# Kernel optimization log

Hardware: AMD Instinct MI355X
Metric: run time of the kernel (lower is better)

Reference implementation:

```python
import jax, jax.numpy as jnp
import numpy as np

N = 50000
C_IN = 64
C_OUT = 64
K = 16
EPS = 1e-5


def _bn(x, g, b, m, v):
    # eval-mode BatchNorm1d over last dim
    return (x - m) * jax.lax.rsqrt(v + EPS) * g + b


def setup_inputs() -> dict:
    key = jax.random.key(0)
    ks = jax.random.split(key, 24)
    def lin(i, fan_in, fan_out):
        s = 1.0 / np.sqrt(fan_in)
        W = jax.random.uniform(ks[i], (fan_in, fan_out), jnp.float32, -s, s)
        b = jax.random.uniform(ks[i + 1], (fan_out,), jnp.float32, -s, s)
        return W, b
    Wq, bq = lin(0, C_IN, C_OUT)
    Wk, bk = lin(2, C_IN, C_OUT)
    Wv, bv = lin(4, C_IN, C_OUT)
    Wp, b_p = lin(6, 3, C_OUT)
    Wg1, bg1 = lin(8, C_OUT, C_OUT)
    Wg2, bg2 = lin(10, C_OUT, C_OUT)
    Wo, bo = lin(12, C_OUT, C_OUT)
    def bn_params(i):
        g = jax.random.uniform(ks[i], (C_OUT,), jnp.float32, 0.5, 1.5)
        b = jax.random.normal(ks[i + 1], (C_OUT,), jnp.float32) * 0.1
        m = jax.random.normal(ks[i + 2], (C_OUT,), jnp.float32) * 0.1
        v = jax.random.uniform(ks[i + 3], (C_OUT,), jnp.float32, 0.5, 1.5)
        return g, b, m, v
    bnp_g, bnp_b, bnp_m, bnp_v = bn_params(14)
    bng_g, bng_b, bng_m, bng_v = bn_params(18)
    points = jax.random.normal(ks[22], (N, 3), jnp.float32)
    features = jax.random.normal(ks[23], (N, C_IN), jnp.float32)
    grouped_indices = jax.random.randint(jax.random.fold_in(key, 7), (N, K), 0, N, jnp.int64 if jax.config.jax_enable_x64 else jnp.int32)
    return dict(points=points, features=features, grouped_indices=grouped_indices,
                Wq=Wq, bq=bq, Wk=Wk, bk=bk, Wv=Wv, bv=bv, Wp=Wp, b_p=b_p,
                bnp_g=bnp_g, bnp_b=bnp_b, bnp_m=bnp_m, bnp_v=bnp_v,
                Wg1=Wg1, bg1=bg1, bng_g=bng_g, bng_b=bng_b, bng_m=bng_m, bng_v=bng_v,
                Wg2=Wg2, bg2=bg2, Wo=Wo, bo=bo)


def reference(points, features, grouped_indices,
              Wq, bq, Wk, bk, Wv, bv, Wp, b_p,
              bnp_g, bnp_b, bnp_m, bnp_v,
              Wg1, bg1, bng_g, bng_b, bng_m, bng_v,
              Wg2, bg2, Wo, bo):
    q = features @ Wq + bq                      # (N, C)
    k = features @ Wk + bk
    v = features @ Wv + bv
    gpts = points[grouped_indices]              # (N, K, 3) gather
    gk = k[grouped_indices]                     # (N, K, C)
    gv = v[grouped_indices]                     # (N, K, C)
    rel = gpts - points[:, None, :]             # (N, K, 3)
    p = jax.nn.relu(_bn(rel @ Wp + b_p, bnp_g, bnp_b, bnp_m, bnp_v))  # (N, K, C)
    a = q[:, None, :] - gk + p                  # (N, K, C)
    h = jax.nn.relu(_bn(a @ Wg1 + bg1, bng_g, bng_b, bng_m, bng_v)) @ Wg2 + bg2
    attn = jax.nn.softmax(h, axis=1)            # softmax over neighbor axis
    out = jnp.sum((gv + p) * attn, axis=1) @ Wo + bo  # (N, C)
    return out
```

## Files before the change

### kernel.cpp

```cpp
#include <hip/hip_runtime.h>
#include <hip/hip_bf16.h>

#define EPSV 1e-5f
#define TW 4
#define TPW 8
#define SPD 76
#define WPD 68

typedef __attribute__((ext_vector_type(8))) short s8v;
typedef __attribute__((ext_vector_type(8))) unsigned short u8v;
typedef __attribute__((ext_vector_type(4))) unsigned short u4v;
typedef __attribute__((ext_vector_type(4))) float f4v;

struct InP {
  const float *points, *features; const int* gidx;
  const float *Wq,*bq,*Wk,*bk,*Wv,*bv,*Wp,*b_p;
  const float *bnp_g,*bnp_b,*bnp_m,*bnp_v;
  const float *Wg1,*bg1,*bng_g,*bng_b,*bng_m,*bng_v;
  const float *Wg2,*bg2,*Wo,*bo;
  float* out; int N;
};
struct WS {
  unsigned short *qW1;
  unsigned short *kvT;
  unsigned short *WAf, *Wkf, *Wvf, *W1f, *W2f, *Wof;
  unsigned short *Wpf;
  float *bq1F, *bpF, *bk1F;
};

__device__ __forceinline__ unsigned short f2bf(float x){
  __hip_bfloat16 h = __float2bfloat16(x);
  unsigned short u; __builtin_memcpy(&u, &h, 2); return u;
}
__device__ __forceinline__ float bf2f(unsigned short s){
  union{unsigned u; float f;} c; c.u = ((unsigned)s) << 16; return c.f;
}
__device__ __forceinline__ unsigned pk2(float x, float y){
  __hip_bfloat162 h = __float22bfloat162_rn(make_float2(x, y));
  unsigned u; __builtin_memcpy(&u, &h, 4); return u;
}
__device__ __forceinline__ s8v pack8(f4v x0, f4v x1){
  s8v r;
  ((unsigned*)&r)[0] = pk2(x0[0], x0[1]);
  ((unsigned*)&r)[1] = pk2(x0[2], x0[3]);
  ((unsigned*)&r)[2] = pk2(x1[0], x1[1]);
  ((unsigned*)&r)[3] = pk2(x1[2], x1[3]);
  return r;
}

__global__ void __launch_bounds__(256) prep_kernel(InP P, WS W){
  __shared__ __align__(16) float sWg1[64*WPD];
  __shared__ __align__(16) float sWq [64*WPD];
  __shared__ __align__(16) float sWk [64*WPD];
  const int tid = threadIdx.x;
  {
    int r = tid >> 2, c0 = (tid & 3) * 16;
    const f4v* g1 = (const f4v*)(P.Wg1 + r*64 + c0);
    const f4v* gq = (const f4v*)(P.Wq  + r*64 + c0);
    const f4v* gk = (const f4v*)(P.Wk  + r*64 + c0);
    f4v* d1 = (f4v*)(sWg1 + r*WPD + c0);
    f4v* dq = (f4v*)(sWq  + r*WPD + c0);
    f4v* dk = (f4v*)(sWk  + r*WPD + c0);
    #pragma unroll
    for (int u = 0; u < 4; u++){ d1[u] = g1[u]; dq[u] = gq[u]; dk[u] = gk[u]; }
  }
  __syncthreads();

  const int g = blockIdx.x*256 + tid;
  const int e = g >> 3, j = g & 7;
  const int f = e >> 6, L = e & 63;
  const int ks = f & 1, nt = f >> 1;
  const int n = nt*16 + (L & 15);
  const int k = ks*32 + ((L >> 4) << 3) + j;
  const float sg = P.bng_g[n] * rsqrtf(P.bng_v[n] + EPSV);
  W.W1f[e*8+j] = f2bf(sWg1[k*WPD+n] * sg);
  W.W2f[e*8+j] = f2bf(P.Wg2[k*64+n]);
  W.Wof[e*8+j] = f2bf(P.Wo [k*64+n]);
  W.Wvf[e*8+j] = f2bf(P.Wv [k*64+n]);
  float acc = 0.f, acck = 0.f;
  #pragma unroll 8
  for (int d = 0; d < 64; d++){
    float w1 = sWg1[d*WPD+n];
    acc  += sWq[k*WPD+d] * w1;
    acck += sWk[k*WPD+d] * w1;
  }
  W.WAf[e*8+j] = f2bf(acc  * sg);
  W.Wkf[e*8+j] = f2bf(acck * sg);
  if (g < 2048){
    int ep = g >> 3;
    int ntp = ep >> 6, Lp = ep & 63;
    int np_ = ntp*16 + (Lp & 15);
    int kp = ((Lp >> 4) << 3) + j;
    float sp = P.bnp_g[np_] * rsqrtf(P.bnp_v[np_] + EPSV);
    W.Wpf[ep*8+j] = f2bf(kp < 3 ? P.Wp[kp*64+np_]*sp : 0.f);
  }
  if (g < 64){
    float sgt = P.bng_g[g] * rsqrtf(P.bng_v[g] + EPSV);
    float spt = P.bnp_g[g] * rsqrtf(P.bnp_v[g] + EPSV);
    float acc2 = 0.f, acck2 = 0.f;
    for (int d = 0; d < 64; d++){
      float w1 = sWg1[d*WPD+g];
      acc2  += P.bq[d] * w1;
      acck2 += P.bk[d] * w1;
    }
    W.bq1F[g] = acc2*sgt + P.bg1[g]*sgt + P.bng_b[g] - P.bng_m[g]*sgt;
    W.bk1F[g] = acck2*sgt;
    W.bpF[g]  = P.b_p[g]*spt + P.bnp_b[g] - P.bnp_m[g]*spt;
  }
}

__global__ void __launch_bounds__(256) qkv_kernel(InP P, WS W){
  const int tid = threadIdx.x;
  const int wid = tid >> 6, l = tid & 63;
  const int cl = l & 15, q = l >> 4;
  const int TILES = (P.N + 15) >> 4;
  const int task = blockIdx.x * TW + wid;
  if (task >= TILES) return;
  const int i0 = task * 16;
  int row = i0 + cl; if (row > P.N - 1) row = P.N - 1;
  const float* fr = P.features + (size_t)row*64 + q*8;
  f4v x0 = *(const f4v*)fr;
  f4v x1 = *(const f4v*)(fr + 4);
  s8v fa0 = pack8(x0, x1);
  x0 = *(const f4v*)(fr + 32);
  x1 = *(const f4v*)(fr + 36);
  s8v fa1 = pack8(x0, x1);

  auto comp = [&](const unsigned short* Bf_, const float* biasPtr, f4v* c){
    const s8v* Bf = (const s8v*)Bf_;
    #pragma unroll
    for (int nt = 0; nt < 4; nt++){
      float bn = biasPtr[nt*16 + cl];
      f4v ci = { bn, bn, bn, bn };
      c[nt] = __builtin_amdgcn_mfma_f32_16x16x32_bf16(fa0, Bf[(2*nt+0)*64 + l], ci, 0, 0, 0);
      c[nt] = __builtin_amdgcn_mfma_f32_16x16x32_bf16(fa1, Bf[(2*nt+1)*64 + l], c[nt], 0, 0, 0);
    }
  };
  f4v qc[4], kc[4], vc[4];
  comp(W.WAf, W.bq1F, qc);
  comp(W.Wkf, W.bk1F, kc);
  comp(W.Wvf, P.bv,   vc);

  #pragma unroll
  for (int r = 0; r < 4; r++){
    int rg = i0 + q*4 + r;
    if (rg < P.N){
      u4v qv;
      qv[0] = f2bf(qc[0][r]); qv[1] = f2bf(qc[1][r]);
      qv[2] = f2bf(qc[2][r]); qv[3] = f2bf(qc[3][r]);
      *(u4v*)(W.qW1 + (size_t)rg*64 + cl*4) = qv;
      u8v kv;
      kv[0] = f2bf(kc[0][r]); kv[1] = f2bf(kc[1][r]);
      kv[2] = f2bf(kc[2][r]); kv[3] = f2bf(kc[3][r]);
      kv[4] = f2bf(vc[0][r]); kv[5] = f2bf(vc[1][r]);
      kv[6] = f2bf(vc[2][r]); kv[7] = f2bf(vc[3][r]);
      *(u8v*)(W.kvT + (size_t)rg*128 + cl*8) = kv;
    }
  }
}

__global__ void __launch_bounds__(256, 2) main_kernel(InP P, WS W){
  __shared__ __align__(16) unsigned short Sp[TW][2][16*SPD];
  __shared__ __align__(16) unsigned short PreB[TW][TPW*SPD];
  __shared__ __align__(16) int sI[TW][TPW*16];
  __shared__ __align__(16) unsigned short sW1[8*64*8];
  __shared__ __align__(16) unsigned short sW2[8*64*8];
  const int tid = threadIdx.x;
  const int wid = tid >> 6, l = tid & 63;
  const int cl = l & 15, q = l >> 4;
  const int TILES = (P.N + TPW - 1) / TPW;
  const int task = blockIdx.x * TW + wid;

  {
    const int4* s1 = (const int4*)W.W1f;
    const int4* s2 = (const int4*)W.W2f;
    ((int4*)sW1)[tid]       = s1[tid];
    ((int4*)sW1)[tid + 256] = s1[tid + 256];
    ((int4*)sW2)[tid]       = s2[tid];
    ((int4*)sW2)[tid + 256] = s2[tid + 256];
  }
  __syncthreads();
  if (task >= TILES) return;
  const int i0 = task * TPW;
  unsigned short* PreBw = PreB[wid];
  int* sIw = sI[wid];
  const s8v* W1s = (const s8v*)sW1;
  const s8v* W2s = (const s8v*)sW2;

  {
    long base = (long)i0*16 + l*2;
    long maxb = (long)P.N*16 - 2;
    if (base > maxb) base = maxb;
    int2 gi = *(const int2*)(P.gidx + base);
    *(int2*)&sIw[l*2] = gi;
  }

  s8v wpf[4];
  {
    const s8v* Wpp = (const s8v*)W.Wpf;
    #pragma unroll
    for (int f = 0; f < 4; f++) wpf[f] = Wpp[f*64 + l];
  }
  float bp4[4], b24[4];
  #pragma unroll
  for (int nt = 0; nt < 4; nt++){ bp4[nt] = W.bpF[nt*16 + cl]; b24[nt] = P.bg2[nt*16 + cl]; }

  float ngx=0.f, ngy=0.f, ngz=0.f;
  {
    int nidx = sIw[cl];
    if (l < 16){ const float* gp = P.points + (size_t)nidx*3; ngx=gp[0]; ngy=gp[1]; ngz=gp[2]; }
  }
  float ncx = P.points[(size_t)i0*3+0];
  float ncy = P.points[(size_t)i0*3+1];
  float ncz = P.points[(size_t)i0*3+2];
  float nq0, nq1, nq2, nq3;
  {
    u4v qv = *(const u4v*)(W.qW1 + (size_t)i0*64 + cl*4);
    nq0 = bf2f(qv[0]); nq1 = bf2f(qv[1]); nq2 = bf2f(qv[2]); nq3 = bf2f(qv[3]);
  }

  int zro = 0;

  #pragma unroll 2
  for (int pt = 0; pt < TPW; pt++){
    asm volatile("" : "+v"(zro));
    unsigned short* Spw = Sp[wid][pt & 1];
    float gx=ngx, gy=ngy, gz=ngz, cx=ncx, cy=ncy, cz=ncz;
    float qcn4[4] = { nq0, nq1, nq2, nq3 };
    const bool valid = (i0 + pt < P.N);

    u8v kv8[4];
    {
      int4 vidx = *(const int4*)&sIw[pt*16 + q*4];
      #pragma unroll
      for (int r = 0; r < 4; r++)
        kv8[r] = *(const u8v*)(W.kvT + (size_t)vidx[r]*128 + cl*8);
    }

    s8v ap;
    ((unsigned*)&ap)[0] = pk2(gx-cx, gy-cy);
    ((unsigned*)&ap)[1] = pk2(gz-cz, 0.f);
    ((unsigned*)&ap)[2] = 0u; ((unsigned*)&ap)[3] = 0u;
    f4v pc[4];
    #pragma unroll
    for (int nt = 0; nt < 4; nt++){
      f4v ci = { bp4[nt], bp4[nt], bp4[nt], bp4[nt] };
      pc[nt] = __builtin_amdgcn_mfma_f32_16x16x32_bf16(ap, wpf[nt], ci, 0, 0, 0);
    }
    #pragma unroll
    for (int nt = 0; nt < 4; nt++){
      #pragma unroll
      for (int r = 0; r < 4; r++){
        pc[nt][r] = fmaxf(pc[nt][r], 0.f);
        Spw[(q*4+r)*SPD + nt*16 + cl] = f2bf(pc[nt][r]);
      }
    }

    {
      int np = (pt + 1) & (TPW-1);
      int nidx = sIw[np*16 + cl];
      if (l < 16){ const float* gp = P.points + (size_t)nidx*3; ngx=gp[0]; ngy=gp[1]; ngz=gp[2]; }
      int ii = i0 + np; if (ii > P.N - 1) ii = P.N - 1;
      ncx = P.points[(size_t)ii*3+0];
      ncy = P.points[(size_t)ii*3+1];
      ncz = P.points[(size_t)ii*3+2];
      u4v qv = *(const u4v*)(W.qW1 + (size_t)ii*64 + cl*4);
      nq0 = bf2f(qv[0]); nq1 = bf2f(qv[1]); nq2 = bf2f(qv[2]); nq3 = bf2f(qv[3]);
    }

    s8v af0 = *(const s8v*)&Spw[cl*SPD + q*8];
    s8v af1 = *(const s8v*)&Spw[cl*SPD + 32 + q*8];

    f4v tc[4];
    #pragma unroll
    for (int nt = 0; nt < 4; nt++){
      f4v ci = { qcn4[nt] - bf2f((unsigned short)kv8[0][nt]),
                 qcn4[nt] - bf2f((unsigned short)kv8[1][nt]),
                 qcn4[nt] - bf2f((unsigned short)kv8[2][nt]),
                 qcn4[nt] - bf2f((unsigned short)kv8[3][nt]) };
      s8v b0 = W1s[(2*nt+0)*64 + l + zro];
      s8v b1 = W1s[(2*nt+1)*64 + l + zro];
      tc[nt] = __builtin_amdgcn_mfma_f32_16x16x32_bf16(af0, b0, ci, 0, 0, 0);
      tc[nt] = __builtin_amdgcn_mfma_f32_16x16x32_bf16(af1, b1, tc[nt], 0, 0, 0);
      #pragma unroll
      for (int r = 0; r < 4; r++) tc[nt][r] = fmaxf(tc[nt][r], 0.f);
    }

    #pragma unroll
    for (int nt = 0; nt < 4; nt++)
      #pragma unroll
      for (int r = 0; r < 4; r++)
        Spw[(q*4+r)*SPD + nt*16 + cl] = f2bf(tc[nt][r]);
    s8v tf0 = *(const s8v*)&Spw[cl*SPD + q*8];
    s8v tf1 = *(const s8v*)&Spw[cl*SPD + 32 + q*8];

    f4v hc[4];
    #pragma unroll
    for (int nt = 0; nt < 4; nt++){
      f4v ci = { b24[nt], b24[nt], b24[nt], b24[nt] };
      s8v b0 = W2s[(2*nt+0)*64 + l + zro];
      s8v b1 = W2s[(2*nt+1)*64 + l + zro];
      hc[nt] = __builtin_amdgcn_mfma_f32_16x16x32_bf16(tf0, b0, ci, 0, 0, 0);
      hc[nt] = __builtin_amdgcn_mfma_f32_16x16x32_bf16(tf1, b1, hc[nt], 0, 0, 0);
    }

    float pre4[4];
    #pragma unroll
    for (int nt = 0; nt < 4; nt++){
      float s = 0.f, acc = 0.f;
      #pragma unroll
      for (int r = 0; r < 4; r++){
        float e2 = __expf(hc[nt][r]);
        s += e2;
        acc = fmaf(e2, bf2f((unsigned short)kv8[r][4+nt]) + pc[nt][r], acc);
      }
      s += __shfl_xor(s, 16, 64);
      s += __shfl_xor(s, 32, 64);
      acc += __shfl_xor(acc, 16, 64);
      acc += __shfl_xor(acc, 32, 64);
      pre4[nt] = acc * __builtin_amdgcn_rcpf(s);
    }
    if (valid){
      float sa = (l & 16) ? pre4[1] : pre4[0];
      float sb = (l & 16) ? pre4[3] : pre4[2];
      PreBw[pt*SPD + l] = f2bf((l & 32) ? sb : sa);
    }
  }

  s8v wof[8];
  {
    const s8v* Wop = (const s8v*)W.Wof;
    #pragma unroll
    for (int f = 0; f < 8; f++) wof[f] = Wop[f*64 + l];
  }
  s8v ef0 = *(const s8v*)&PreBw[(cl & (TPW-1))*SPD + q*8];
  s8v ef1 = *(const s8v*)&PreBw[(cl & (TPW-1))*SPD + 32 + q*8];
  #pragma unroll
  for (int nt = 0; nt < 4; nt++){
    float bn = P.bo[nt*16 + cl];
    f4v ci = { bn, bn, bn, bn };
    f4v oc = __builtin_amdgcn_mfma_f32_16x16x32_bf16(ef0, wof[2*nt+0], ci, 0, 0, 0);
    oc = __builtin_amdgcn_mfma_f32_16x16x32_bf16(ef1, wof[2*nt+1], oc, 0, 0, 0);
    #pragma unroll
    for (int r = 0; r < 4; r++){
      int ro = q*4 + r;
      int rg = i0 + ro;
      if (ro < TPW && rg < P.N) P.out[(size_t)rg*64 + nt*16 + cl] = oc[r];
    }
  }
}

extern "C" void kernel_launch(void* const* d_in, const int* in_sizes, int n_in,
                              void* d_out, int out_size, void* d_ws, size_t ws_size,
                              hipStream_t stream){
  InP P;
  P.points   = (const float*)d_in[0];
  P.features = (const float*)d_in[1];
  P.gidx     = (const int*)d_in[2];
  P.Wq  = (const float*)d_in[3];  P.bq  = (const float*)d_in[4];
  P.Wk  = (const float*)d_in[5];  P.bk  = (const float*)d_in[6];
  P.Wv  = (const float*)d_in[7];  P.bv  = (const float*)d_in[8];
  P.Wp  = (const float*)d_in[9];  P.b_p = (const float*)d_in[10];
  P.bnp_g = (const float*)d_in[11]; P.bnp_b = (const float*)d_in[12];
  P.bnp_m = (const float*)d_in[13]; P.bnp_v = (const float*)d_in[14];
  P.Wg1 = (const float*)d_in[15]; P.bg1 = (const float*)d_in[16];
  P.bng_g = (const float*)d_in[17]; P.bng_b = (const float*)d_in[18];
  P.bng_m = (const float*)d_in[19]; P.bng_v = (const float*)d_in[20];
  P.Wg2 = (const float*)d_in[21]; P.bg2 = (const float*)d_in[22];
  P.Wo  = (const float*)d_in[23]; P.bo  = (const float*)d_in[24];
  P.out = (float*)d_out;
  const int N = in_sizes[0] / 3;
  P.N = N;

  WS W;
  char* w = (char*)d_ws;
  W.qW1 = (unsigned short*)w; w += (size_t)N*64*2;
  W.kvT = (unsigned short*)w; w += (size_t)N*128*2;
  W.WAf = (unsigned short*)w; w += 8*64*8*2;
  W.Wkf = (unsigned short*)w; w += 8*64*8*2;
  W.Wvf = (unsigned short*)w; w += 8*64*8*2;
  W.W1f = (unsigned short*)w; w += 8*64*8*2;
  W.W2f = (unsigned short*)w; w += 8*64*8*2;
  W.Wof = (unsigned short*)w; w += 8*64*8*2;
  W.Wpf = (unsigned short*)w; w += 4*64*8*2;
  W.bq1F = (float*)w; w += 256;
  W.bpF  = (float*)w; w += 256;
  W.bk1F = (float*)w; w += 256;

  const int TILES16 = (N + 15) / 16;
  const int grid16 = (TILES16 + TW - 1) / TW;
  const int TILESM = (N + TPW - 1) / TPW;
  const int gridM = (TILESM + TW - 1) / TW;
  hipLaunchKernelGGL(prep_kernel, dim3(16),     dim3(256), 0, stream, P, W);
  hipLaunchKernelGGL(qkv_kernel,  dim3(grid16), dim3(256), 0, stream, P, W);
  hipLaunchKernelGGL(main_kernel, dim3(gridM),  dim3(256), 0, stream, P, W);
}
```

Baseline: 196.7 us.

## Process two points per iteration to interleave independent MFMA chains

Restructures the per-wave point loop to handle two points (A and B) per iteration. Their gathers, position-encoding MFMAs, MLP MFMAs and softmax reductions are interleaved, and the prefetch covers the next two points. The aim is to hide MFMA dependency latency and gather latency by exposing more independent work. In exchange it roughly doubles live registers, which may cut occupancy or cause spills. The initial prefetch of point i0+1 is not clamped to N.

```diff
diff --git a/kernel.cpp b/kernel.cpp
--- a/kernel.cpp
+++ b/kernel.cpp
@@ -205,125 +205,177 @@
   #pragma unroll
   for (int nt = 0; nt < 4; nt++){ bp4[nt] = W.bpF[nt*16 + cl]; b24[nt] = P.bg2[nt*16 + cl]; }
 
-  float ngx=0.f, ngy=0.f, ngz=0.f;
-  {
-    int nidx = sIw[cl];
-    if (l < 16){ const float* gp = P.points + (size_t)nidx*3; ngx=gp[0]; ngy=gp[1]; ngz=gp[2]; }
-  }
-  float ncx = P.points[(size_t)i0*3+0];
-  float ncy = P.points[(size_t)i0*3+1];
-  float ncz = P.points[(size_t)i0*3+2];
-  float nq0, nq1, nq2, nq3;
-  {
-    u4v qv = *(const u4v*)(W.qW1 + (size_t)i0*64 + cl*4);
-    nq0 = bf2f(qv[0]); nq1 = bf2f(qv[1]); nq2 = bf2f(qv[2]); nq3 = bf2f(qv[3]);
+  float nAgx=0.f,nAgy=0.f,nAgz=0.f, nBgx=0.f,nBgy=0.f,nBgz=0.f;
+  {
+    if (l < 16){
+      int na = sIw[cl];        const float* ga = P.points + (size_t)na*3;
+      nAgx=ga[0]; nAgy=ga[1]; nAgz=ga[2];
+      int nb = sIw[16 + cl];   const float* gb = P.points + (size_t)nb*3;
+      nBgx=gb[0]; nBgy=gb[1]; nBgz=gb[2];
+    }
+  }
+  float nAcx = P.points[(size_t)i0*3+0], nAcy = P.points[(size_t)i0*3+1], nAcz = P.points[(size_t)i0*3+2];
+  float nBcx = P.points[(size_t)(i0+1)*3+0], nBcy = P.points[(size_t)(i0+1)*3+1], nBcz = P.points[(size_t)(i0+1)*3+2];
+  float nAq0,nAq1,nAq2,nAq3, nBq0,nBq1,nBq2,nBq3;
+  {
+    u4v qa = *(const u4v*)(W.qW1 + (size_t)i0*64 + cl*4);
+    nAq0=bf2f(qa[0]); nAq1=bf2f(qa[1]); nAq2=bf2f(qa[2]); nAq3=bf2f(qa[3]);
+    u4v qb = *(const u4v*)(W.qW1 + (size_t)(i0+1)*64 + cl*4);
+    nBq0=bf2f(qb[0]); nBq1=bf2f(qb[1]); nBq2=bf2f(qb[2]); nBq3=bf2f(qb[3]);
   }
 
   int zro = 0;
 
-  #pragma unroll 2
-  for (int pt = 0; pt < TPW; pt++){
+  #pragma unroll 1
+  for (int pt = 0; pt < TPW; pt += 2){
     asm volatile("" : "+v"(zro));
-    unsigned short* Spw = Sp[wid][pt & 1];
-    float gx=ngx, gy=ngy, gz=ngz, cx=ncx, cy=ncy, cz=ncz;
-    float qcn4[4] = { nq0, nq1, nq2, nq3 };
-    const bool valid = (i0 + pt < P.N);
-
-    u8v kv8[4];
+    unsigned short* SpA = Sp[wid][0];
+    unsigned short* SpB = Sp[wid][1];
+    float gxA=nAgx, gyA=nAgy, gzA=nAgz, cxA=nAcx, cyA=nAcy, czA=nAcz;
+    float gxB=nBgx, gyB=nBgy, gzB=nBgz, cxB=nBcx, cyB=nBcy, czB=nBcz;
+    float qA4[4] = { nAq0, nAq1, nAq2, nAq3 };
+    float qB4[4] = { nBq0, nBq1, nBq2, nBq3 };
+    const bool vA = (i0 + pt     < P.N);
+    const bool vB = (i0 + pt + 1 < P.N);
+
+    u8v kvA[4], kvB[4];
     {
-      int4 vidx = *(const int4*)&sIw[pt*16 + q*4];
-      #pragma unroll
-      for (int r = 0; r < 4; r++)
-        kv8[r] = *(const u8v*)(W.kvT + (size_t)vidx[r]*128 + cl*8);
-    }
-
-    s8v ap;
-    ((unsigned*)&ap)[0] = pk2(gx-cx, gy-cy);
-    ((unsigned*)&ap)[1] = pk2(gz-cz, 0.f);
-    ((unsigned*)&ap)[2] = 0u; ((unsigned*)&ap)[3] = 0u;
-    f4v pc[4];
+      int4 via = *(const int4*)&sIw[pt*16 + q*4];
+      int4 vib = *(const int4*)&sIw[(pt+1)*16 + q*4];
+      #pragma unroll
+      for (int r = 0; r < 4; r++){
+        kvA[r] = *(const u8v*)(W.kvT + (size_t)via[r]*128 + cl*8);
+        kvB[r] = *(const u8v*)(W.kvT + (size_t)vib[r]*128 + cl*8);
+      }
+    }
+
+    f4v pcA[4], pcB[4];
+    {
+      s8v apA, apB;
+      ((unsigned*)&apA)[0] = pk2(gxA-cxA, gyA-cyA);
+      ((unsigned*)&apA)[1] = pk2(gzA-czA, 0.f);
+      ((unsigned*)&apA)[2] = 0u; ((unsigned*)&apA)[3] = 0u;
+      ((unsigned*)&apB)[0] = pk2(gxB-cxB, gyB-cyB);
+      ((unsigned*)&apB)[1] = pk2(gzB-czB, 0.f);
+      ((unsigned*)&apB)[2] = 0u; ((unsigned*)&apB)[3] = 0u;
+      #pragma unroll
+      for (int nt = 0; nt < 4; nt++){
+        f4v ci = { bp4[nt], bp4[nt], bp4[nt], bp4[nt] };
+        pcA[nt] = __builtin_amdgcn_mfma_f32_16x16x32_bf16(apA, wpf[nt], ci, 0, 0, 0);
+        pcB[nt] = __builtin_amdgcn_mfma_f32_16x16x32_bf16(apB, wpf[nt], ci, 0, 0, 0);
+      }
+      #pragma unroll
+      for (int nt = 0; nt < 4; nt++){
+        #pragma unroll
+        for (int r = 0; r < 4; r++){
+          pcA[nt][r] = fmaxf(pcA[nt][r], 0.f);
+          pcB[nt][r] = fmaxf(pcB[nt][r], 0.f);
+          SpA[(q*4+r)*SPD + nt*16 + cl] = f2bf(pcA[nt][r]);
+          SpB[(q*4+r)*SPD + nt*16 + cl] = f2bf(pcB[nt][r]);
+        }
+      }
+    }
+
+    {
+      int np2 = (pt + 2) & (TPW-1), np3 = (pt + 3) & (TPW-1);
+      if (l < 16){
+        int na = sIw[np2*16 + cl]; const float* ga = P.points + (size_t)na*3;
+        nAgx=ga[0]; nAgy=ga[1]; nAgz=ga[2];
+        int nb = sIw[np3*16 + cl]; const float* gb = P.points + (size_t)nb*3;
+        nBgx=gb[0]; nBgy=gb[1]; nBgz=gb[2];
+      }
+      int iA = i0 + np2; if (iA > P.N - 1) iA = P.N - 1;
+      int iB = i0 + np3; if (iB > P.N - 1) iB = P.N - 1;
+      nAcx = P.points[(size_t)iA*3+0]; nAcy = P.points[(size_t)iA*3+1]; nAcz = P.points[(size_t)iA*3+2];
+      nBcx = P.points[(size_t)iB*3+0]; nBcy = P.points[(size_t)iB*3+1]; nBcz = P.points[(size_t)iB*3+2];
+      u4v qa = *(const u4v*)(W.qW1 + (size_t)iA*64 + cl*4);
+      nAq0=bf2f(qa[0]); nAq1=bf2f(qa[1]); nAq2=bf2f(qa[2]); nAq3=bf2f(qa[3]);
+      u4v qb = *(const u4v*)(W.qW1 + (size_t)iB*64 + cl*4);
+      nBq0=bf2f(qb[0]); nBq1=bf2f(qb[1]); nBq2=bf2f(qb[2]); nBq3=bf2f(qb[3]);
+    }
+
+    s8v afA0 = *(const s8v*)&SpA[cl*SPD + q*8];
+    s8v afA1 = *(const s8v*)&SpA[cl*SPD + 32 + q*8];
+    s8v afB0 = *(const s8v*)&SpB[cl*SPD + q*8];
+    s8v afB1 = *(const s8v*)&SpB[cl*SPD + 32 + q*8];
+
+    f4v tcA[4], tcB[4];
     #pragma unroll
     for (int nt = 0; nt < 4; nt++){
-      f4v ci = { bp4[nt], bp4[nt], bp4[nt], bp4[nt] };
-      pc[nt] = __builtin_amdgcn_mfma_f32_16x16x32_bf16(ap, wpf[nt], ci, 0, 0, 0);
-    }
-    #pragma unroll
-    for (int nt = 0; nt < 4; nt++){
-      #pragma unroll
-      for (int r = 0; r < 4; r++){
-        pc[nt][r] = fmaxf(pc[nt][r], 0.f);
-        Spw[(q*4+r)*SPD + nt*16 + cl] = f2bf(pc[nt][r]);
-      }
-    }
-
-    {
-      int np = (pt + 1) & (TPW-1);
-      int nidx = sIw[np*16 + cl];
-      if (l < 16){ const float* gp = P.points + (size_t)nidx*3; ngx=gp[0]; ngy=gp[1]; ngz=gp[2]; }
-      int ii = i0 + np; if (ii > P.N - 1) ii = P.N - 1;
-      ncx = P.points[(size_t)ii*3+0];
-      ncy = P.points[(size_t)ii*3+1];
-      ncz = P.points[(size_t)ii*3+2];
-      u4v qv = *(const u4v*)(W.qW1 + (size_t)ii*64 + cl*4);
-      nq0 = bf2f(qv[0]); nq1 = bf2f(qv[1]); nq2 = bf2f(qv[2]); nq3 = bf2f(qv[3]);
-    }
-
-    s8v af0 = *(const s8v*)&Spw[cl*SPD + q*8];
-    s8v af1 = *(const s8v*)&Spw[cl*SPD + 32 + q*8];
-
-    f4v tc[4];
-    #pragma unroll
-    for (int nt = 0; nt < 4; nt++){
-      f4v ci = { qcn4[nt] - bf2f((unsigned short)kv8[0][nt]),
-                 qcn4[nt] - bf2f((unsigned short)kv8[1][nt]),
-                 qcn4[nt] - bf2f((unsigned short)kv8[2][nt]),
-                 qcn4[nt] - bf2f((unsigned short)kv8[3][nt]) };
+      f4v ciA = { qA4[nt] - bf2f((unsigned short)kvA[0][nt]),
+                  qA4[nt] - bf2f((unsigned short)kvA[1][nt]),
+                  qA4[nt] - bf2f((unsigned short)kvA[2][nt]),
+                  qA4[nt] - bf2f((unsigned short)kvA[3][nt]) };
+      f4v ciB = { qB4[nt] - bf2f((unsigned short)kvB[0][nt]),
+                  qB4[nt] - bf2f((unsigned short)kvB[1][nt]),
+                  qB4[nt] - bf2f((unsigned short)kvB[2][nt]),
+                  qB4[nt] - bf2f((unsigned short)kvB[3][nt]) };
       s8v b0 = W1s[(2*nt+0)*64 + l + zro];
       s8v b1 = W1s[(2*nt+1)*64 + l + zro];
-      tc[nt] = __builtin_amdgcn_mfma_f32_16x16x32_bf16(af0, b0, ci, 0, 0, 0);
-      tc[nt] = __builtin_amdgcn_mfma_f32_16x16x32_bf16(af1, b1, tc[nt], 0, 0, 0);
-      #pragma unroll
-      for (int r = 0; r < 4; r++) tc[nt][r] = fmaxf(tc[nt][r], 0.f);
+      tcA[nt] = __builtin_amdgcn_mfma_f32_16x16x32_bf16(afA0, b0, ciA, 0, 0, 0);
+      tcA[nt] = __builtin_amdgcn_mfma_f32_16x16x32_bf16(afA1, b1, tcA[nt], 0, 0, 0);
+      tcB[nt] = __builtin_amdgcn_mfma_f32_16x16x32_bf16(afB0, b0, ciB, 0, 0, 0);
+      tcB[nt] = __builtin_amdgcn_mfma_f32_16x16x32_bf16(afB1, b1, tcB[nt], 0, 0, 0);
+      #pragma unroll
+      for (int r = 0; r < 4; r++){
+        tcA[nt][r] = fmaxf(tcA[nt][r], 0.f);
+        tcB[nt][r] = fmaxf(tcB[nt][r], 0.f);
+      }
     }
 
     #pragma unroll
     for (int nt = 0; nt < 4; nt++)
       #pragma unroll
-      for (int r = 0; r < 4; r++)
-        Spw[(q*4+r)*SPD + nt*16 + cl] = f2bf(tc[nt][r]);
-    s8v tf0 = *(const s8v*)&Spw[cl*SPD + q*8];
-    s8v tf1 = *(const s8v*)&Spw[cl*SPD + 32 + q*8];
-
-    f4v hc[4];
+      for (int r = 0; r < 4; r++){
+        SpA[(q*4+r)*SPD + nt*16 + cl] = f2bf(tcA[nt][r]);
+        SpB[(q*4+r)*SPD + nt*16 + cl] = f2bf(tcB[nt][r]);
+      }
+    s8v tfA0 = *(const s8v*)&SpA[cl*SPD + q*8];
+    s8v tfA1 = *(const s8v*)&SpA[cl*SPD + 32 + q*8];
+    s8v tfB0 = *(const s8v*)&SpB[cl*SPD + q*8];
+    s8v tfB1 = *(const s8v*)&SpB[cl*SPD + 32 + q*8];
+
+    f4v hcA[4], hcB[4];
     #pragma unroll
     for (int nt = 0; nt < 4; nt++){
       f4v ci = { b24[nt], b24[nt], b24[nt], b24[nt] };
       s8v b0 = W2s[(2*nt+0)*64 + l + zro];
       s8v b1 = W2s[(2*nt+1)*64 + l + zro];
-      hc[nt] = __builtin_amdgcn_mfma_f32_16x16x32_bf16(tf0, b0, ci, 0, 0, 0);
-      hc[nt] = __builtin_amdgcn_mfma_f32_16x16x32_bf16(tf1, b1, hc[nt], 0, 0, 0);
-    }
-
-    float pre4[4];
+      hcA[nt] = __builtin_amdgcn_mfma_f32_16x16x32_bf16(tfA0, b0, ci, 0, 0, 0);
+      hcA[nt] = __builtin_amdgcn_mfma_f32_16x16x32_bf16(tfA1, b1, hcA[nt], 0, 0, 0);
+      hcB[nt] = __builtin_amdgcn_mfma_f32_16x16x32_bf16(tfB0, b0, ci, 0, 0, 0);
+      hcB[nt] = __builtin_amdgcn_mfma_f32_16x16x32_bf16(tfB1, b1, hcB[nt], 0, 0, 0);
+    }
+
+    float preA[4], preB4[4];
     #pragma unroll
     for (int nt = 0; nt < 4; nt++){
-      float s = 0.f, acc = 0.f;
+      float sA = 0.f, aA = 0.f, sB = 0.f, aB = 0.f;
       #pragma unroll
       for (int r = 0; r < 4; r++){
-        float e2 = __expf(hc[nt][r]);
-        s += e2;
-        acc = fmaf(e2, bf2f((unsigned short)kv8[r][4+nt]) + pc[nt][r], acc);
-      }
-      s += __shfl_xor(s, 16, 64);
-      s += __shfl_xor(s, 32, 64);
-      acc += __shfl_xor(acc, 16, 64);
-      acc += __shfl_xor(acc, 32, 64);
-      pre4[nt] = acc * __builtin_amdgcn_rcpf(s);
-    }
-    if (valid){
-      float sa = (l & 16) ? pre4[1] : pre4[0];
-      float sb = (l & 16) ? pre4[3] : pre4[2];
+        float eA = __expf(hcA[nt][r]);
+        sA += eA;
+        aA = fmaf(eA, bf2f((unsigned short)kvA[r][4+nt]) + pcA[nt][r], aA);
+        float eB = __expf(hcB[nt][r]);
+        sB += eB;
+        aB = fmaf(eB, bf2f((unsigned short)kvB[r][4+nt]) + pcB[nt][r], aB);
+      }
+      sA += __shfl_xor(sA, 16, 64); sB += __shfl_xor(sB, 16, 64);
+      sA += __shfl_xor(sA, 32, 64); sB += __shfl_xor(sB, 32, 64);
+      aA += __shfl_xor(aA, 16, 64); aB += __shfl_xor(aB, 16, 64);
+      aA += __shfl_xor(aA, 32, 64); aB += __shfl_xor(aB, 32, 64);
+      preA[nt]  = aA * __builtin_amdgcn_rcpf(sA);
+      preB4[nt] = aB * __builtin_amdgcn_rcpf(sB);
+    }
+    if (vA){
+      float sa = (l & 16) ? preA[1] : preA[0];
+      float sb = (l & 16) ? preA[3] : preA[2];
       PreBw[pt*SPD + l] = f2bf((l & 32) ? sb : sa);
+    }
+    if (vB){
+      float sa = (l & 16) ? preB4[1] : preB4[0];
+      float sb = (l & 16) ? preB4[3] : preB4[2];
+      PreBw[(pt+1)*SPD + l] = f2bf((l & 32) ? sb : sa);
     }
   }
 
```

After: 202.5 us. +2.9%, slower.
